# Optimization experiments

Hardware: AMD Instinct MI355X
Metric: run time of the kernel (lower is better)

## Reference

```python
import jax, jax.numpy as jnp
import numpy as np

SR = 16000
FREQ_POINTS = 2 * SR          # IR length / FFT size
NBINS = FREQ_POINTS // 2 + 1  # rfft bins
D = 8                         # delay lines
AP = 4                        # allpass sections per line
EARLY_LEN = 200


def setup_inputs() -> dict:
    key = jax.random.key(0)
    ks = jax.random.split(key, 9)
    return {
        "audio_dry": jax.random.normal(ks[0], (4, 1, 32000), jnp.float32),
        "early_ir": 0.1 * jax.random.normal(ks[1], (EARLY_LEN,), jnp.float32),
        "input_gain": 0.25 + 0.1 * jax.random.normal(ks[2], (D,), jnp.float32),
        "output_gain": 0.25 + 0.1 * jax.random.normal(ks[3], (D,), jnp.float32),
        # keep strictly positive / away from 0 for numerical sanity (torch init clamps at 0)
        "time_rev_0_sec": jnp.abs(0.1 * jax.random.normal(ks[4], (1,), jnp.float32)) + 0.3,
        "alpha_tone": jnp.abs(0.1 * jax.random.normal(ks[5], (1,), jnp.float32)) + 0.5,
        "delay_values": 400.0 + 60.0 * jax.random.normal(ks[6], (D,), jnp.float32),
        "delays_allpass": 400.0 + 60.0 * jax.random.normal(ks[7], (D, AP), jnp.float32),
        "gain_allpass": 0.25 + 0.1 * jax.random.normal(ks[8], (D, AP), jnp.float32),
    }


def _get_ir(early_ir, input_gain, output_gain, time_rev_0_sec, alpha_tone,
            delay_values, delays_allpass, gain_allpass):
    wk = 2.0 * jnp.pi * jnp.arange(NBINS, dtype=jnp.float32) / FREQ_POINTS  # [F]
    zk = jnp.exp(-1j * wk)  # e^{-j w_k}, [F] complex64

    # Fractional delay: integer delay * 1st-order allpass interpolator -> diag of delay matrix
    z_d = jnp.exp(-1j * (wk[:, None] * jnp.floor(delay_values)[None, :]))      # [F, D]
    d_eta = delay_values - jnp.floor(delay_values)
    eta = (1.0 - d_eta) / (1.0 + d_eta)                                        # [D]
    ap_interp = (eta[None, :] + zk[:, None]) / (1.0 + eta[None, :] * zk[:, None])
    d_vec = (z_d * ap_interp).astype(jnp.complex64)                            # [F, D]

    # One-pole absorption filters (diag of filter matrix)
    t0 = time_rev_0_sec[0]
    alpha = alpha_tone[0]
    delay_sec = (delay_values + jnp.sum(delays_allpass, axis=-1)) / SR         # [D]
    k = jnp.power(10.0, -3.0 * delay_sec / t0)
    kpi = jnp.power(10.0, -3.0 * delay_sec / (alpha * t0))
    g = 2.0 * k * kpi / (k + kpi)
    p = (k - kpi) / (k + kpi)
    filt = g[None, :] / (1.0 - p[None, :] * zk[:, None] + 1e-8)               # [F, D]

    # Allpass decorrelators: product of AP sections per line (diag)
    z_delays = jnp.exp(1j * (wk[:, None, None] * delays_allpass[None]))        # [F, D, AP]
    ga = gain_allpass[None].astype(jnp.complex64)
    ap_tf = jnp.prod((1.0 + ga * z_delays) / (ga + z_delays), axis=-1)         # [F, D]

    # feedback = diag(filt) @ M @ diag(ap_tf)  (diagonal scaling instead of diag_embed+matmul)
    M = (-jnp.eye(D, dtype=jnp.float32) + 0.5 * jnp.ones((D, D), jnp.float32)).astype(jnp.complex64)
    feedback = filt[:, :, None] * M[None] * ap_tf[:, None, :]                  # [F, D, D]

    # H(w) = out_g . diag(d) (I - feedback diag(d))^{-1} in_g   (solve instead of explicit inv)
    A = jnp.eye(D, dtype=jnp.complex64)[None] - feedback * d_vec[:, None, :]   # [F, D, D]
    b = jnp.broadcast_to(input_gain.astype(jnp.complex64), (NBINS, D))[..., None]
    x = jnp.linalg.solve(A, b)[..., 0]                                         # [F, D]
    transfer = jnp.einsum('fd,fd->f', d_vec * x, jnp.broadcast_to(output_gain.astype(jnp.complex64), (NBINS, D)))

    late_ir = jnp.fft.irfft(transfer, n=FREQ_POINTS).astype(jnp.float32)       # [FREQ_POINTS]
    return late_ir.at[:EARLY_LEN].add(early_ir)


def reference(audio_dry, early_ir, input_gain, output_gain, time_rev_0_sec,
              alpha_tone, delay_values, delays_allpass, gain_allpass):
    ir = _get_ir(early_ir, input_gain, output_gain, time_rev_0_sec, alpha_tone,
                 delay_values, delays_allpass, gain_allpass)
    K = ir.shape[0]
    left = (K - 1) // 2
    right = (K - 1) - left  # torch conv1d padding='same' (cross-correlation, extra pad on right)
    out = jax.lax.conv_general_dilated(
        audio_dry, ir[None, None, :], window_strides=(1,),
        padding=[(left, right)], dimension_numbers=('NCH', 'OIH', 'NCH'))
    return out[:, 0, :]  # [B, T]
```

## Files before the change

kernel.cpp:

```cpp
#include <hip/hip_runtime.h>

#define N_FFT 32000
#define NBINS 16001
#define NDL 8
#define NAP 4
#define EARLY_LEN 200
#define T_LEN 32000
#define NB 4

#define ASTRIDE 65600
#define APAD 16000

#define KSPLIT 32
#define KRANGE 512
#define KTOT   16384
#define OB 4096
#define WSPAN 4576
#define XPHYS 5184
#define HS_ROW_L 536
#define HWLEN 544

struct c32 { float re, im; };

__device__ __forceinline__ c32 cmul(c32 a, c32 b) {
    return { a.re*b.re - a.im*b.im, a.re*b.im + a.im*b.re };
}
__device__ __forceinline__ c32 cdiv(c32 a, c32 b) {
    float inv = 1.0f / (b.re*b.re + b.im*b.im);
    return { (a.re*b.re + a.im*b.im)*inv, (a.im*b.re - a.re*b.im)*inv };
}

typedef _Float16 f16x8 __attribute__((ext_vector_type(8)));
typedef float    f32x16 __attribute__((ext_vector_type(16)));

__device__ __forceinline__ float h2f(unsigned short u) {
    return (float)__builtin_bit_cast(_Float16, u);
}
__device__ __forceinline__ unsigned short f2h(float f) {
    return __builtin_bit_cast(unsigned short, (_Float16)f);
}

__global__ __launch_bounds__(512) void stageAT_kernel(
    const float* __restrict__ ing, const float* __restrict__ outg,
    const float* __restrict__ t0p, const float* __restrict__ alphap,
    const float* __restrict__ delays, const float* __restrict__ dap,
    const float* __restrict__ gap, float2* __restrict__ G,
    const float* __restrict__ audio, unsigned short* __restrict__ audio_h)
{
    __shared__ float2 sxA[129];
    __shared__ float2 tab[256];
    __shared__ float2 pa[512];
    int tid = threadIdx.x;
    int k1 = blockIdx.x;

    if (k1 >= 125) {
        int i4 = (k1 - 125) * 512 + tid;
        if (i4 >= NB * (ASTRIDE/8)) return;
        int b = i4 / (ASTRIDE/8);
        int q = i4 - b * (ASTRIDE/8);
        int u0 = q * 8 - APAD;
        unsigned r[4];
        if (u0 >= 0 && u0 + 8 <= T_LEN) {
            const float4* ap = (const float4*)(audio + b*T_LEN + u0);
            float4 v0 = ap[0], v1 = ap[1];
            r[0] = f2h(v0.x) | ((unsigned)f2h(v0.y) << 16);
            r[1] = f2h(v0.z) | ((unsigned)f2h(v0.w) << 16);
            r[2] = f2h(v1.x) | ((unsigned)f2h(v1.y) << 16);
            r[3] = f2h(v1.z) | ((unsigned)f2h(v1.w) << 16);
        } else {
            unsigned short hh[8];
            #pragma unroll
            for (int e = 0; e < 8; e++) {
                int u = u0 + e;
                float v = (u >= 0 && u < T_LEN) ? audio[b*T_LEN + u] : 0.0f;
                hh[e] = f2h(v);
            }
            r[0] = hh[0] | ((unsigned)hh[1] << 16);
            r[1] = hh[2] | ((unsigned)hh[3] << 16);
            r[2] = hh[4] | ((unsigned)hh[5] << 16);
            r[3] = hh[6] | ((unsigned)hh[7] << 16);
        }
        ((uint4*)audio_h)[i4] = make_uint4(r[0], r[1], r[2], r[3]);
        return;
    }

    if (tid < 256) {
        float c, s;
        sincosf(2.4544246578366045e-02f * (float)tid, &s, &c);
        tab[tid] = make_float2(c, s);
    }

    const float  TWf = 1.9634954084936207e-04f;
    const double TWd = 1.9634954084936207740e-04;
    float t0v = t0p[0], alpha = alphap[0];

    for (int base = 0; base < 1032; base += 512) {
        int task = base + tid;
        if (task >= 1032) break;
        int k2 = task >> 3, d = task & 7;
        int f = k1 + 125 * k2;
        if (f > 16000) { if (d == 0) sxA[k2] = make_float2(0.f, 0.f); continue; }

        float wk = TWf * (float)f;
        float cwk, swk;
        sincosf(wk, &swk, &cwk);

        float dval = delays[d];
        float fid = floorf(dval);
        float d_eta = dval - fid;
        float eta = (1.0f - d_eta) / (1.0f + d_eta);
        long long mm = ((long long)f * (long long)fid) % N_FFT;
        float a0 = TWf * (float)mm;
        float c0, s0; sincosf(a0, &s0, &c0);
        c32 z_d = { c0, -s0 };
        c32 num = { eta + cwk, -swk };
        c32 den = { 1.0f + eta*cwk, -eta*swk };
        c32 dvec = cmul(z_d, cdiv(num, den));

        float dsum = dval;
        #pragma unroll
        for (int a = 0; a < NAP; a++) dsum += dap[d*NAP + a];
        float delay_sec = dsum * (1.0f/16000.0f);
        float kf  = expf(-3.0f*delay_sec/t0v * 2.3025850929940457f);
        float kpi = expf(-3.0f*delay_sec/(alpha*t0v) * 2.3025850929940457f);
        float g = 2.0f*kf*kpi/(kf+kpi);
        float p = (kf - kpi)/(kf + kpi);
        c32 fden = { 1.0f + 1e-8f - p*cwk, p*swk };
        c32 filt = cdiv({g, 0.f}, fden);

        c32 ap = {1.f, 0.f};
        #pragma unroll
        for (int a = 0; a < NAP; a++) {
            float dl = dap[d*NAP + a];
            double ph = fmod((double)f * (double)dl, (double)N_FFT);
            float aa = (float)(ph * TWd);
            float ca, sa; sincosf(aa, &sa, &ca);
            float ga = gap[d*NAP + a];
            c32 nume = { 1.0f + ga*ca, ga*sa };
            c32 dene = { ga + ca, sa };
            ap = cmul(ap, cdiv(nume, dene));
        }
        c32 cd = cmul(ap, dvec);
        c32 rc = cmul(filt, cd);
        c32 Dd = { 1.0f + rc.re, rc.im };
        c32 invD = cdiv({1.f, 0.f}, Dd);
        float bg = ing[d];
        c32 t1 = cmul({cd.re*bg, cd.im*bg}, invD);
        c32 t2 = cmul(rc, invD);
        float s1r = t1.re, s1i = t1.im, s2r = t2.re, s2i = t2.im;
        #pragma unroll
        for (int msk = 1; msk < 8; msk <<= 1) {
            s1r += __shfl_xor(s1r, msk);
            s1i += __shfl_xor(s1i, msk);
            s2r += __shfl_xor(s2r, msk);
            s2i += __shfl_xor(s2i, msk);
        }
        c32 denl = { 1.0f - 0.5f*s2r, -0.5f*s2i };
        c32 lam = cdiv({0.5f*s1r, 0.5f*s1i}, denl);
        c32 lr = cmul(lam, filt);
        c32 xv = cmul(invD, {bg + lr.re, lr.im});
        c32 term = cmul(dvec, xv);
        float og = outg[d];
        float trr = term.re * og, tri = term.im * og;
        #pragma unroll
        for (int msk = 1; msk < 8; msk <<= 1) {
            trr += __shfl_xor(trr, msk);
            tri += __shfl_xor(tri, msk);
        }
        if (d == 0) {
            float w = (f == 0 || f == 16000) ? 0.5f : 1.0f;
            sxA[k2] = make_float2(trr * w, tri * w);
        }
    }
    __syncthreads();

    {
        int r = tid & 255, half = tid >> 8;
        int k2s = half ? 65 : 0, k2e = half ? 129 : 65;
        float ar = 0.f, ai = 0.f;
        int p = (k2s * r) & 255;
        for (int k2 = k2s; k2 < k2e; k2++) {
            float2 X = sxA[k2];
            float2 E = tab[p];
            ar = fmaf(X.x, E.x, fmaf(-X.y, E.y, ar));
            ai = fmaf(X.x, E.y, fmaf( X.y, E.x, ai));
            p = (p + r) & 255;
        }
        pa[tid] = make_float2(ar, ai);
    }
    __syncthreads();
    if (tid < 256) {
        float2 a = pa[tid], b = pa[tid + 256];
        G[k1 * 256 + tid] = make_float2(a.x + b.x, a.y + b.y);
    }
}

__global__ __launch_bounds__(512) void stageB_kernel(
    const float2* __restrict__ G, const float* __restrict__ early,
    unsigned short* __restrict__ h_g)
{
    const float TWf = 1.9634954084936207e-04f;
    int n   = blockIdx.x * 64 + (threadIdx.x >> 3);
    int sub = threadIdx.x & 7;
    int k10 = sub * 16;
    int nk1 = (sub == 7) ? 13 : 16;

    int m0 = (n * k10) % N_FFT;
    float er, ei; sincosf(TWf * (float)m0, &ei, &er);
    float wc, wss; sincosf(TWf * (float)n, &wss, &wc);

    float ar = 0.f;
    const float2* gp = G + (n & 255) + k10 * 256;
    #pragma unroll 4
    for (int k = 0; k < nk1; k++) {
        float2 g = gp[k * 256];
        ar = fmaf(g.x, er, fmaf(-g.y, ei, ar));
        float nr = fmaf(er, wc, -(ei*wss));
        float ni = fmaf(er, wss,  (ei*wc));
        er = nr; ei = ni;
    }
    ar += __shfl_xor(ar, 1);
    ar += __shfl_xor(ar, 2);
    ar += __shfl_xor(ar, 4);
    if (sub == 0) {
        float v = ar * (2.0f / (float)N_FFT);
        if (n < EARLY_LEN) v += early[n];
        h_g[n] = f2h(v);
    }
}

__global__ __launch_bounds__(512) void conv_mfma_kernel(
    const unsigned short* __restrict__ audio_h,
    const unsigned short* __restrict__ h_g,
    unsigned short* __restrict__ pconv)
{
    __shared__ __attribute__((aligned(16))) char Sraw[2*XPHYS*2 + 32*HS_ROW_L*2 + HWLEN*2];
    _Float16* xs = (_Float16*)Sraw;
    _Float16* hs = (_Float16*)(Sraw + 2*XPHYS*2);
    _Float16* hw = (_Float16*)(Sraw + 2*XPHYS*2 + 32*HS_ROW_L*2);
    float*    red = (float*)Sraw;

    int tid = threadIdx.x;
    int lane = tid & 63;
    int w = tid >> 6;
    int bb = w & 1;
    int tq = (w >> 1) & 1;
    int kw = w >> 2;
    int bx = blockIdx.x, bp = blockIdx.y, kz = blockIdx.z;
    int t0 = bx * OB;
    int b0g = bp * 2;
    int K0 = kz * KRANGE;
    int wbase = t0 + K0;

    const uint4* xg = (const uint4*)audio_h;
    for (int q = tid; q < 2 * (WSPAN/8); q += 512) {
        int bbs = (q >= WSPAN/8) ? 1 : 0;
        int qq = q - (WSPAN/8) * bbs;
        uint4 v = xg[(size_t)(b0g + bbs) * (ASTRIDE/8) + (wbase >> 3) + qq];
        ((uint4*)xs)[bbs * (XPHYS/8) + qq + (qq >> 3)] = v;
    }
    {
        unsigned* hw32 = (unsigned*)hw;
        const unsigned* hg32 = (const unsigned*)h_g;
        int sbase = (K0 - 32) >> 1;
        for (int j2 = tid; j2 < HWLEN/2; j2 += 512)
            hw32[j2] = (sbase + j2 >= 0) ? hg32[sbase + j2] : 0u;
    }
    __syncthreads();

    {
        const unsigned short* hwu = (const unsigned short*)hw;
        int i  = tid & 31;
        int q0 = tid >> 5;
        #pragma unroll
        for (int e = 0; e < 4; e++) {
            int q = q0 + 16 * e;
            int src = 8 * q - i + 31;
            unsigned o[4];
            #pragma unroll
            for (int j = 0; j < 4; j++)
                o[j] = (unsigned)hwu[src + 2*j] | ((unsigned)hwu[src + 2*j + 1] << 16);
            *(uint4*)(hs + i * HS_ROW_L + 8 * q) = make_uint4(o[0], o[1], o[2], o[3]);
        }
    }
    __syncthreads();

    int l31 = lane & 31, g = lane >> 5;
    int aBase = l31 * HS_ROW_L + 8 * g;
    int pB0 = 1024 * (2*tq + 0) + 32 * l31 + 8 * g;
    int pB1 = 1024 * (2*tq + 1) + 32 * l31 + 8 * g;
    const _Float16* xb = xs + (bb ? XPHYS : 0);

    f32x16 acc0 = {0,0,0,0,0,0,0,0,0,0,0,0,0,0,0,0};
    f32x16 acc1 = {0,0,0,0,0,0,0,0,0,0,0,0,0,0,0,0};
    #pragma unroll 4
    for (int ksl = 0; ksl < 16; ksl++) {
        int ksg = kw * 16 + ksl;
        f16x8 af = *(const f16x8*)(hs + aBase + 16 * ksg);
        int p0 = pB0 + 16 * ksg;
        int p1 = pB1 + 16 * ksg;
        f16x8 bf0 = *(const f16x8*)(xb + p0 + 8 * (p0 >> 6));
        f16x8 bf1 = *(const f16x8*)(xb + p1 + 8 * (p1 >> 6));
        acc0 = __builtin_amdgcn_mfma_f32_32x32x16_f16(af, bf0, acc0, 0, 0, 0);
        acc1 = __builtin_amdgcn_mfma_f32_32x32x16_f16(af, bf1, acc1, 0, 0, 0);
    }
    __syncthreads();
    int slot0 = ((bb * 2 + tq) * 2 + 0) * 1024;
    int slot1 = ((bb * 2 + tq) * 2 + 1) * 1024;
    if (kw == 1) {
        #pragma unroll
        for (int r = 0; r < 16; r++) {
            red[slot0 + r * 64 + lane] = acc0[r];
            red[slot1 + r * 64 + lane] = acc1[r];
        }
    }
    __syncthreads();
    if (kw == 0) {
        unsigned short* po = pconv + (size_t)(kz * NB + b0g + bb) * T_LEN;
        #pragma unroll
        for (int s = 0; s < 2; s++) {
            int T = 2 * tq + s;
            int slot = s ? slot1 : slot0;
            #pragma unroll
            for (int r = 0; r < 16; r += 2) {
                float v0 = (s ? acc1[r]   : acc0[r])   + red[slot + r * 64 + lane];
                float v1 = (s ? acc1[r+1] : acc0[r+1]) + red[slot + (r+1) * 64 + lane];
                int i = (r & 3) + 8 * (r >> 2) + 4 * g;
                int t = t0 + 1024 * T + i + 32 * l31;
                if (t < T_LEN) {
                    unsigned u = f2h(v0) | ((unsigned)f2h(v1) << 16);
                    *(unsigned*)(po + t) = u;
                }
            }
        }
    }
}

__global__ void finish_kernel(const unsigned short* __restrict__ pconv,
                              float* __restrict__ out)
{
    int i = blockIdx.x * 256 + threadIdx.x;
    if (i >= NB * T_LEN) return;
    float s = 0.f;
    #pragma unroll
    for (int kz = 0; kz < KSPLIT; kz++)
        s += h2f(pconv[(size_t)kz * NB * T_LEN + i]);
    out[i] = s;
}

extern "C" void kernel_launch(void* const* d_in, const int* in_sizes, int n_in,
                              void* d_out, int out_size, void* d_ws, size_t ws_size,
                              hipStream_t stream) {
    const float* audio  = (const float*)d_in[0];
    const float* early  = (const float*)d_in[1];
    const float* ing    = (const float*)d_in[2];
    const float* outg   = (const float*)d_in[3];
    const float* t0p    = (const float*)d_in[4];
    const float* alphap = (const float*)d_in[5];
    const float* delays = (const float*)d_in[6];
    const float* dap    = (const float*)d_in[7];
    const float* gap    = (const float*)d_in[8];

    char* ws = (char*)d_ws;
    float2*         G       = (float2*)(ws);
    unsigned short* h_g     = (unsigned short*)(ws + 262144);
    unsigned short* audio_h = (unsigned short*)(ws + 294912);
    unsigned short* pconv   = (unsigned short*)(ws + 819712);

    stageAT_kernel<<<190, 512, 0, stream>>>(ing, outg, t0p, alphap,
                                            delays, dap, gap, G,
                                            audio, audio_h);
    stageB_kernel<<<256, 512, 0, stream>>>(G, early, h_g);
    conv_mfma_kernel<<<dim3(8, 2, KSPLIT), 512, 0, stream>>>(audio_h, h_g, pconv);
    finish_kernel<<<500, 256, 0, stream>>>(pconv, (float*)d_out);
}
```

Before: 41.63 us.

## Halve K-split and reduce partial convolutions with float atomics into output

```diff
diff --git a/kernel.cpp b/kernel.cpp
--- a/kernel.cpp
+++ b/kernel.cpp
@@ -11,14 +11,13 @@
 #define ASTRIDE 65600
 #define APAD 16000
 
-#define KSPLIT 32
-#define KRANGE 512
+#define KSPLIT 16
+#define KRANGE 1024
 #define KTOT   16384
 #define OB 4096
-#define WSPAN 4576
-#define XPHYS 5184
-#define HS_ROW_L 536
-#define HWLEN 544
+#define WSPAN 5088
+#define XPHYS 5760
+#define HS_ROW_L 1048
 
 struct c32 { float re, im; };
 
@@ -45,7 +44,8 @@
     const float* __restrict__ t0p, const float* __restrict__ alphap,
     const float* __restrict__ delays, const float* __restrict__ dap,
     const float* __restrict__ gap, float2* __restrict__ G,
-    const float* __restrict__ audio, unsigned short* __restrict__ audio_h)
+    const float* __restrict__ audio, unsigned short* __restrict__ audio_h,
+    float* __restrict__ out)
 {
     __shared__ float2 sxA[129];
     __shared__ float2 tab[256];
@@ -55,6 +55,8 @@
 
     if (k1 >= 125) {
         int i4 = (k1 - 125) * 512 + tid;
+        if (i4 < NB * T_LEN / 4)
+            ((float4*)out)[i4] = make_float4(0.f, 0.f, 0.f, 0.f);
         if (i4 >= NB * (ASTRIDE/8)) return;
         int b = i4 / (ASTRIDE/8);
         int q = i4 - b * (ASTRIDE/8);
@@ -232,9 +234,9 @@
 __global__ __launch_bounds__(512) void conv_mfma_kernel(
     const unsigned short* __restrict__ audio_h,
     const unsigned short* __restrict__ h_g,
-    unsigned short* __restrict__ pconv)
+    float* __restrict__ out)
 {
-    __shared__ __attribute__((aligned(16))) char Sraw[2*XPHYS*2 + 32*HS_ROW_L*2 + HWLEN*2];
+    __shared__ __attribute__((aligned(16))) char Sraw[2*XPHYS*2 + 32*HS_ROW_L*2 + 1056*2];
     _Float16* xs = (_Float16*)Sraw;
     _Float16* hs = (_Float16*)(Sraw + 2*XPHYS*2);
     _Float16* hw = (_Float16*)(Sraw + 2*XPHYS*2 + 32*HS_ROW_L*2);
@@ -252,6 +254,13 @@
     int K0 = kz * KRANGE;
     int wbase = t0 + K0;
 
+    {
+        unsigned* hw32 = (unsigned*)hw;
+        const unsigned* hg32 = (const unsigned*)h_g;
+        int sbase = (K0 - 32) >> 1;
+        for (int j2 = tid; j2 < 528; j2 += 512)
+            hw32[j2] = (sbase + j2 >= 0) ? hg32[sbase + j2] : 0u;
+    }
     const uint4* xg = (const uint4*)audio_h;
     for (int q = tid; q < 2 * (WSPAN/8); q += 512) {
         int bbs = (q >= WSPAN/8) ? 1 : 0;
@@ -259,13 +268,6 @@
         uint4 v = xg[(size_t)(b0g + bbs) * (ASTRIDE/8) + (wbase >> 3) + qq];
         ((uint4*)xs)[bbs * (XPHYS/8) + qq + (qq >> 3)] = v;
     }
-    {
-        unsigned* hw32 = (unsigned*)hw;
-        const unsigned* hg32 = (const unsigned*)h_g;
-        int sbase = (K0 - 32) >> 1;
-        for (int j2 = tid; j2 < HWLEN/2; j2 += 512)
-            hw32[j2] = (sbase + j2 >= 0) ? hg32[sbase + j2] : 0u;
-    }
     __syncthreads();
 
     {
@@ -273,7 +275,7 @@
         int i  = tid & 31;
         int q0 = tid >> 5;
         #pragma unroll
-        for (int e = 0; e < 4; e++) {
+        for (int e = 0; e < 8; e++) {
             int q = q0 + 16 * e;
             int src = 8 * q - i + 31;
             unsigned o[4];
@@ -294,8 +296,8 @@
     f32x16 acc0 = {0,0,0,0,0,0,0,0,0,0,0,0,0,0,0,0};
     f32x16 acc1 = {0,0,0,0,0,0,0,0,0,0,0,0,0,0,0,0};
     #pragma unroll 4
-    for (int ksl = 0; ksl < 16; ksl++) {
-        int ksg = kw * 16 + ksl;
+    for (int ksl = 0; ksl < 32; ksl++) {
+        int ksg = kw * 32 + ksl;
         f16x8 af = *(const f16x8*)(hs + aBase + 16 * ksg);
         int p0 = pB0 + 16 * ksg;
         int p1 = pB1 + 16 * ksg;
@@ -316,7 +318,7 @@
     }
     __syncthreads();
     if (kw == 0) {
-        unsigned short* po = pconv + (size_t)(kz * NB + b0g + bb) * T_LEN;
+        float* po = out + (size_t)(b0g + bb) * T_LEN;
         #pragma unroll
         for (int s = 0; s < 2; s++) {
             int T = 2 * tq + s;
@@ -328,24 +330,12 @@
                 int i = (r & 3) + 8 * (r >> 2) + 4 * g;
                 int t = t0 + 1024 * T + i + 32 * l31;
                 if (t < T_LEN) {
-                    unsigned u = f2h(v0) | ((unsigned)f2h(v1) << 16);
-                    *(unsigned*)(po + t) = u;
+                    atomicAdd(po + t, v0);
+                    atomicAdd(po + t + 1, v1);
                 }
             }
         }
     }
-}
-
-__global__ void finish_kernel(const unsigned short* __restrict__ pconv,
-                              float* __restrict__ out)
-{
-    int i = blockIdx.x * 256 + threadIdx.x;
-    if (i >= NB * T_LEN) return;
-    float s = 0.f;
-    #pragma unroll
-    for (int kz = 0; kz < KSPLIT; kz++)
-        s += h2f(pconv[(size_t)kz * NB * T_LEN + i]);
-    out[i] = s;
 }
 
 extern "C" void kernel_launch(void* const* d_in, const int* in_sizes, int n_in,
@@ -365,12 +355,10 @@
     float2*         G       = (float2*)(ws);
     unsigned short* h_g     = (unsigned short*)(ws + 262144);
     unsigned short* audio_h = (unsigned short*)(ws + 294912);
-    unsigned short* pconv   = (unsigned short*)(ws + 819712);
 
     stageAT_kernel<<<190, 512, 0, stream>>>(ing, outg, t0p, alphap,
                                             delays, dap, gap, G,
-                                            audio, audio_h);
+                                            audio, audio_h, (float*)d_out);
     stageB_kernel<<<256, 512, 0, stream>>>(G, early, h_g);
-    conv_mfma_kernel<<<dim3(8, 2, KSPLIT), 512, 0, stream>>>(audio_h, h_g, pconv);
-    finish_kernel<<<500, 256, 0, stream>>>(pconv, (float*)d_out);
-}
+    conv_mfma_kernel<<<dim3(8, 2, KSPLIT), 512, 0, stream>>>(audio_h, h_g, (float*)d_out);
+}
```

Measured after the change: 111.8 us. 2.69x slower.
